# Performance work log

Measured on AMD Instinct MI355X. Metric: run time of the kernel, lower is better.

Reference implementation:

```python
import jax, jax.numpy as jnp
import numpy as np

N_NODES = 50000
N_EDGES = 400000
N_GRAPHS = 256
D = 200
N_STEPS = 6


def setup_inputs() -> dict:
    key = jax.random.key(0)
    ks = jax.random.split(key, 10)
    s = 1.0 / np.sqrt(D)
    x = jax.random.normal(ks[0], (N_NODES, D), dtype=jnp.float32)
    edge_index = jax.random.randint(ks[1], (2, N_EDGES), 0, N_NODES, dtype=jnp.int64)
    batch = jnp.sort(jax.random.randint(ks[2], (N_NODES,), 0, N_GRAPHS, dtype=jnp.int64))
    ggnn_weight = jax.random.uniform(ks[3], (N_STEPS, D, D), jnp.float32, -s, s)
    w_ih = jax.random.uniform(ks[4], (3 * D, D), jnp.float32, -s, s)
    w_hh = jax.random.uniform(ks[5], (3 * D, D), jnp.float32, -s, s)
    b_ih = jax.random.uniform(ks[6], (3 * D,), jnp.float32, -s, s)
    b_hh = jax.random.uniform(ks[7], (3 * D,), jnp.float32, -s, s)
    cls_w = jax.random.uniform(ks[8], (2, D), jnp.float32, -s, s)
    cls_b = jax.random.uniform(ks[9], (2,), jnp.float32, -s, s)
    return {"x": x, "edge_index": edge_index, "batch": batch,
            "ggnn_weight": ggnn_weight, "w_ih": w_ih, "w_hh": w_hh,
            "b_ih": b_ih, "b_hh": b_hh, "cls_w": cls_w, "cls_b": cls_b}


def _gru_cell(m, h, w_ih, w_hh, b_ih, b_hh):
    gi = m @ w_ih.T + b_ih            # [N, 3D]
    gh = h @ w_hh.T + b_hh            # [N, 3D]
    i_r, i_z, i_n = jnp.split(gi, 3, axis=-1)
    h_r, h_z, h_n = jnp.split(gh, 3, axis=-1)
    r = jax.nn.sigmoid(i_r + h_r)
    z = jax.nn.sigmoid(i_z + h_z)
    n = jnp.tanh(i_n + r * h_n)
    return (1.0 - z) * n + z * h


def reference(x, edge_index, batch, ggnn_weight, w_ih, w_hh, b_ih, b_hh, cls_w, cls_b):
    src, dst = edge_index[0], edge_index[1]

    def step(h, W):
        m = h @ W                                        # [N, D]
        agg = jax.ops.segment_sum(m[src], dst, num_segments=N_NODES)  # scatter-add
        return _gru_cell(agg, h, w_ih, w_hh, b_ih, b_hh), None

    h, _ = jax.lax.scan(step, x, ggnn_weight)
    h = jax.nn.relu(h)
    pooled = jax.ops.segment_max(h, batch, num_segments=N_GRAPHS)    # [G, D]
    logits = pooled @ cls_w.T + cls_b                                # [G, 2]
    return jax.nn.sigmoid(logits)
```

## Files before the change

### kernel.cpp

```cpp
#include <hip/hip_runtime.h>
#include <cstdint>
#include <cstddef>

#define NN 50000
#define NE 400000
#define NG 256
#define DIM 200
#define NSTEPS 6

typedef unsigned int uint;
typedef unsigned short ushort;
typedef __attribute__((ext_vector_type(8))) short short8;
typedef __attribute__((ext_vector_type(4))) float f32x4;

#define GLL16(gsrc, ldst)                                                        \
  __builtin_amdgcn_global_load_lds(                                              \
      (const __attribute__((address_space(1))) void*)(gsrc),                     \
      (__attribute__((address_space(3))) void*)(ldst), 16, 0, 0)

__device__ __forceinline__ float bfu(ushort u) { return __uint_as_float((uint)u << 16); }
__device__ __forceinline__ uint packf(float v) {
  uint u = __float_as_uint(v);
  uint t = u + 0x7fffu + ((u >> 16) & 1u);
  uint hb = t & 0xffff0000u;
  float lo = v - __uint_as_float(hb);
  uint ul = __float_as_uint(lo);
  uint t2 = ul + 0x7fffu + ((ul >> 16) & 1u);
  return hb | (t2 >> 16);
}
__device__ __forceinline__ uint packf_tr(float v) {
  uint u = __float_as_uint(v);
  uint t = u + 0x7fffu + ((u >> 16) & 1u);
  uint hb = t & 0xffff0000u;
  float lo = v - __uint_as_float(hb);
  return hb | (__float_as_uint(lo) >> 16);
}
__device__ __forceinline__ ushort bf16rn(float v) {
  uint u = __float_as_uint(v);
  return (ushort)((u + 0x7fffu + ((u >> 16) & 1u)) >> 16);
}
__device__ __forceinline__ float fsig(float x) {
  return __builtin_amdgcn_rcpf(1.f + __expf(-x));
}
__device__ __forceinline__ float ftanh(float x) {
  return 1.f - 2.f * __builtin_amdgcn_rcpf(__expf(2.f * x) + 1.f);
}

__global__ void k_zero_i32(int* __restrict__ p, int n) {
  for (int i = blockIdx.x * blockDim.x + threadIdx.x; i < n; i += gridDim.x * blockDim.x)
    p[i] = 0;
}
__global__ void k_zero_f32(float* __restrict__ p, int n) {
  for (int i = blockIdx.x * blockDim.x + threadIdx.x; i < n; i += gridDim.x * blockDim.x)
    p[i] = 0.f;
}
__global__ void k_hist(const int* __restrict__ dst, int* __restrict__ cnt, int nE) {
  int e = blockIdx.x * blockDim.x + threadIdx.x;
  if (e < nE) atomicAdd(&cnt[dst[e]], 1);
}

__global__ __launch_bounds__(256) void k_scan_blk(const int* __restrict__ cnt,
                                                  int* __restrict__ incl,
                                                  int* __restrict__ bsum, int n) {
  __shared__ int buf[256];
  int i = blockIdx.x * 256 + threadIdx.x;
  int v = (i < n) ? cnt[i] : 0;
  buf[threadIdx.x] = v;
  __syncthreads();
#pragma unroll
  for (int d = 1; d < 256; d <<= 1) {
    int t = (threadIdx.x >= d) ? buf[threadIdx.x - d] : 0;
    __syncthreads();
    buf[threadIdx.x] += t;
    __syncthreads();
  }
  if (i < n) incl[i] = buf[threadIdx.x];
  if (threadIdx.x == 255) bsum[blockIdx.x] = buf[255];
}
__global__ __launch_bounds__(256) void k_scan_top(int* __restrict__ bsum, int nb) {
  __shared__ int buf[256];
  int v = (threadIdx.x < nb) ? bsum[threadIdx.x] : 0;
  buf[threadIdx.x] = v;
  __syncthreads();
#pragma unroll
  for (int d = 1; d < 256; d <<= 1) {
    int t = (threadIdx.x >= d) ? buf[threadIdx.x - d] : 0;
    __syncthreads();
    buf[threadIdx.x] += t;
    __syncthreads();
  }
  if (threadIdx.x < nb) bsum[threadIdx.x] = buf[threadIdx.x] - v;
}
__global__ __launch_bounds__(256) void k_scan_fin(const int* __restrict__ cnt,
                                                  const int* __restrict__ incl,
                                                  const int* __restrict__ bsum,
                                                  int* __restrict__ off,
                                                  int* __restrict__ cursor, int n) {
  int i = blockIdx.x * 256 + threadIdx.x;
  if (i < n) {
    int o = incl[i] + bsum[blockIdx.x];
    off[i + 1] = o;
    cursor[i] = o - cnt[i];
  }
  if (i == 0) off[0] = 0;
}

__global__ void k_scatter(const int* __restrict__ dst, const int* __restrict__ src,
                          int* __restrict__ cursor, int* __restrict__ slist, int nE) {
  int e = blockIdx.x * blockDim.x + threadIdx.x;
  if (e < nE) {
    int d = dst[e];
    int pos = atomicAdd(&cursor[d], 1);
    slist[pos] = src[e];
  }
}

__global__ void k_pack_split(const float* __restrict__ x, ushort* __restrict__ hHi,
                             ushort* __restrict__ hLo, int n8) {
  for (int i = blockIdx.x * blockDim.x + threadIdx.x; i < n8;
       i += gridDim.x * blockDim.x) {
    const float* s = x + (size_t)i * 8;
    uint hi[4], lo[4];
#pragma unroll
    for (int j = 0; j < 4; ++j) {
      uint w0 = packf(s[j * 2]), w1 = packf(s[j * 2 + 1]);
      hi[j] = (w0 >> 16) | (w1 & 0xffff0000u);
      lo[j] = (w0 & 0xffffu) | (w1 << 16);
    }
    *reinterpret_cast<uint4*>(hHi + (size_t)i * 8) = make_uint4(hi[0], hi[1], hi[2], hi[3]);
    *reinterpret_cast<uint4*>(hLo + (size_t)i * 8) = make_uint4(lo[0], lo[1], lo[2], lo[3]);
  }
}

__global__ void k_pack_bf(const float* __restrict__ in, ushort* __restrict__ out, int n) {
  for (int i = blockIdx.x * blockDim.x + threadIdx.x; i < n; i += gridDim.x * blockDim.x)
    out[i] = bf16rn(in[i]);
}

#define GBM 64
#define GBN 64
#define GBK 8
__global__ __launch_bounds__(256) void k_gemm_wc(const float* __restrict__ gg,
                                                 const float* __restrict__ w_ih,
                                                 ushort* __restrict__ wcB) {
  __shared__ __align__(16) float As[GBK][GBM];
  __shared__ __align__(16) float Bs[GBK][GBN];
  int s = blockIdx.z;
  const float* A = gg + (size_t)s * DIM * DIM;
  ushort* out = wcB + (size_t)s * 3 * DIM * DIM;
  int tid = threadIdx.x;
  int row0 = blockIdx.y * GBM;
  int col0 = blockIdx.x * GBN;
  int ty = tid >> 4, tx = tid & 15;
  float acc[4][4] = {};
  for (int k0 = 0; k0 < DIM; k0 += GBK) {
    {
      int r = tid >> 2;
      int kk = (tid & 3) * 2;
      int gr = row0 + r;
      float2 v = make_float2(0.f, 0.f);
      if (gr < DIM) v = *reinterpret_cast<const float2*>(&A[(size_t)gr * DIM + k0 + kk]);
      As[kk][r] = v.x; As[kk + 1][r] = v.y;
    }
    {
      int n = tid >> 2;
      int kk = (tid & 3) * 2;
      int gn = col0 + n;
      float2 v = *reinterpret_cast<const float2*>(&w_ih[(size_t)gn * DIM + k0 + kk]);
      Bs[kk][n] = v.x; Bs[kk + 1][n] = v.y;
    }
    __syncthreads();
#pragma unroll
    for (int k = 0; k < GBK; ++k) {
      float4 av = *reinterpret_cast<const float4*>(&As[k][ty * 4]);
      float4 bv = *reinterpret_cast<const float4*>(&Bs[k][tx * 4]);
      float a[4] = {av.x, av.y, av.z, av.w};
      float b[4] = {bv.x, bv.y, bv.z, bv.w};
#pragma unroll
      for (int i = 0; i < 4; ++i)
#pragma unroll
        for (int j = 0; j < 4; ++j) acc[i][j] += a[i] * b[j];
    }
    __syncthreads();
  }
#pragma unroll
  for (int i = 0; i < 4; ++i) {
    int r = row0 + ty * 4 + i;
    if (r >= DIM) continue;
#pragma unroll
    for (int j = 0; j < 4; ++j) {
      int c = col0 + tx * 4 + j;
      out[(size_t)c * DIM + r] = bf16rn(acc[i][j]);
    }
  }
}

__global__ __launch_bounds__(256) void k_aggregate_hi(const ushort* __restrict__ hHi,
                                                      const int* __restrict__ off,
                                                      const int* __restrict__ slist,
                                                      ushort* __restrict__ aggHi) {
  int wid = blockIdx.x * 4 + (threadIdx.x >> 6);
  int half = (threadIdx.x >> 5) & 1;
  int node = wid * 2 + half;
  int lane32 = threadIdx.x & 31;
  bool nok = node < NN;
  bool act = (lane32 < 25) && nok;
  const uint4* hb = reinterpret_cast<const uint4*>(hHi);
  float a[8] = {};
  int beg = 0, end = 0;
  if (nok) { beg = off[node]; end = off[node + 1]; }
  int p = beg;
#define ACC8(q)                                                   \
  {                                                               \
    a[0] += __uint_as_float((q).x << 16);                         \
    a[1] += __uint_as_float((q).x & 0xffff0000u);                 \
    a[2] += __uint_as_float((q).y << 16);                         \
    a[3] += __uint_as_float((q).y & 0xffff0000u);                 \
    a[4] += __uint_as_float((q).z << 16);                         \
    a[5] += __uint_as_float((q).z & 0xffff0000u);                 \
    a[6] += __uint_as_float((q).w << 16);                         \
    a[7] += __uint_as_float((q).w & 0xffff0000u);                 \
  }
  for (; p + 7 < end; p += 8) {
    uint4 q[8];
    if (act) {
#pragma unroll
      for (int e = 0; e < 8; ++e) q[e] = hb[(size_t)slist[p + e] * 25 + lane32];
#pragma unroll
      for (int e = 0; e < 8; ++e) ACC8(q[e])
    }
  }
  for (; p + 3 < end; p += 4) {
    uint4 q[4];
    if (act) {
#pragma unroll
      for (int e = 0; e < 4; ++e) q[e] = hb[(size_t)slist[p + e] * 25 + lane32];
#pragma unroll
      for (int e = 0; e < 4; ++e) ACC8(q[e])
    }
  }
  for (; p < end; ++p) {
    int s = slist[p];
    if (act) {
      uint4 q = hb[(size_t)s * 25 + lane32];
      ACC8(q)
    }
  }
#undef ACC8
  if (act) {
    uint w[4];
#pragma unroll
    for (int j = 0; j < 4; ++j)
      w[j] = (uint)bf16rn(a[j * 2]) | ((uint)bf16rn(a[j * 2 + 1]) << 16);
    reinterpret_cast<uint4*>(aggHi)[(size_t)node * 25 + lane32] =
        make_uint4(w[0], w[1], w[2], w[3]);
  }
}

#define NPAN 391
#define PPC 3
#define NCHK 131
#define NCOLB 7
#define GRIDF 917

#define MFMA16(a, b, c) __builtin_amdgcn_mfma_f32_16x16x32_bf16(a, b, c, 0, 0, 0)

__global__ __launch_bounds__(256, 2) void k_fused_mfma(
    const ushort* __restrict__ aggHi, const ushort* __restrict__ hHi,
    const ushort* __restrict__ hLo,
    const ushort* __restrict__ wcB, const ushort* __restrict__ whB,
    const float* __restrict__ b_ih, const float* __restrict__ b_hh,
    ushort* __restrict__ hnHi, ushort* __restrict__ hnLo) {
  __shared__ uint4 Bb[6][25][32];

  int tid = threadIdx.x;
  int lane = tid & 63;
  int wv = tid >> 6;
  int lr = lane & 15;
  int kc = lane >> 4;

  int x = blockIdx.x & 7, ii = blockIdx.x >> 3;
  int work = (x < 5 ? x * 115 : 575 + (x - 5) * 114) + ii;
  int chunk = work / NCOLB;
  int col = work - chunk * NCOLB;
  int cc0 = col * 32;

  int c0 = cc0 + lr;
  int c1 = c0 + 16;
  bool c0ok = c0 < DIM, c1ok = c1 < DIM;
  int c0c = c0ok ? c0 : DIM - 1;
  int c1c = c1ok ? c1 : DIM - 1;

  float bias[2][6];
#pragma unroll
  for (int ct = 0; ct < 2; ++ct) {
    int c = ct ? c1c : c0c;
    bias[ct][0] = b_ih[c];           bias[ct][1] = b_ih[DIM + c];
    bias[ct][2] = b_ih[2 * DIM + c]; bias[ct][3] = b_hh[c];
    bias[ct][4] = b_hh[DIM + c];     bias[ct][5] = b_hh[2 * DIM + c];
  }

  {
    uint4* BbF = &Bb[0][0][0];
    for (int i2 = 0; i2 < 19; ++i2) {
      int u = tid + i2 * 256;
      if (u < 4800) {
        int mat = u / 800;
        int rem = u - mat * 800;
        int ch = rem >> 5;
        int c = rem & 31;
        int gc = cc0 + c; if (gc > 199) gc = 199;
        const ushort* wsrc = (mat & 1) ? whB : wcB;
        GLL16(wsrc + (size_t)((mat >> 1) * DIM + gc) * DIM + ch * 8, BbF + u);
      }
    }
  }
  __syncthreads();

  for (int j = 0; j < PPC; ++j) {
    int p = chunk * PPC + j;
    if (p >= NPAN) break;
    int prow0 = p * 128;
    int r0 = prow0 + wv * 32 + lr;
    int r1 = r0 + 16;
    int rc0 = r0 < NN ? r0 : NN - 1;
    int rc1 = r1 < NN ? r1 : NN - 1;
    const ushort* a0 = aggHi + (size_t)rc0 * DIM;
    const ushort* a1 = aggHi + (size_t)rc1 * DIM;
    const ushort* h0 = hHi + (size_t)rc0 * DIM;
    const ushort* h1 = hHi + (size_t)rc1 * DIM;

    uint rbase[2][4];
    bool rok[2][4];
#pragma unroll
    for (int rf = 0; rf < 2; ++rf)
#pragma unroll
      for (int qq = 0; qq < 4; ++qq) {
        int r_ = prow0 + wv * 32 + rf * 16 + kc * 4 + qq;
        rok[rf][qq] = r_ < NN;
        rbase[rf][qq] = (uint)(r_ < NN ? r_ : NN - 1) * DIM;
      }

    f32x4 acc[3][2][2][2] = {};
    short8 aq[4][2][2];
    ushort hvh[2][2][4], hvl[2][2][4];

#define LDA(d, t)                                                              \
  {                                                                            \
    const bool v_ = ((t) < 6) || (kc == 0);                                    \
    const int of_ = v_ ? ((t) * 32 + kc * 8) : 0;                              \
    const short8 z_ = {0, 0, 0, 0, 0, 0, 0, 0};                                \
    aq[d][0][0] = v_ ? *reinterpret_cast<const short8*>(a0 + of_) : z_;        \
    aq[d][0][1] = v_ ? *reinterpret_cast<const short8*>(a1 + of_) : z_;        \
    aq[d][1][0] = v_ ? *reinterpret_cast<const short8*>(h0 + of_) : z_;        \
    aq[d][1][1] = v_ ? *reinterpret_cast<const short8*>(h1 + of_) : z_;        \
  }

    LDA(0, 0)
    LDA(1, 1)
    LDA(2, 2)
#pragma unroll
    for (int t = 0; t < 7; ++t) {
      const int cur = t & 3;
      if (t < 4) LDA((t + 3) & 3, t + 3)
      if (t == 5) {
#pragma unroll
        for (int ct = 0; ct < 2; ++ct) {
          int cc = ct ? c1c : c0c;
#pragma unroll
          for (int rf = 0; rf < 2; ++rf)
#pragma unroll
            for (int qq = 0; qq < 4; ++qq) {
              uint base = rbase[rf][qq] + cc;
              hvh[ct][rf][qq] = hHi[base];
              hvl[ct][rf][qq] = hLo[base];
            }
        }
      }
      int bch = t * 4 + kc; if (bch > 24) bch = 24;
      __builtin_amdgcn_s_setprio(1);
#pragma unroll
      for (int g = 0; g < 3; ++g) {
#pragma unroll
        for (int ct = 0; ct < 2; ++ct) {
          short8 b1 = *reinterpret_cast<const short8*>(&Bb[g * 2 + 0][bch][ct * 16 + lr]);
          short8 b2 = *reinterpret_cast<const short8*>(&Bb[g * 2 + 1][bch][ct * 16 + lr]);
#pragma unroll
          for (int rf = 0; rf < 2; ++rf) {
            acc[g][0][rf][ct] = MFMA16(aq[cur][0][rf], b1, acc[g][0][rf][ct]);
            acc[g][1][rf][ct] = MFMA16(aq[cur][1][rf], b2, acc[g][1][rf][ct]);
          }
        }
      }
      __builtin_amdgcn_s_setprio(0);
    }
#undef LDA

#pragma unroll
    for (int ct = 0; ct < 2; ++ct) {
      if (!(ct ? c1ok : c0ok)) continue;
      int cc = ct ? c1 : c0;
#pragma unroll
      for (int rf = 0; rf < 2; ++rf) {
#pragma unroll
        for (int qq = 0; qq < 4; ++qq) {
          if (!rok[rf][qq]) continue;
          uint base = rbase[rf][qq] + cc;
          float gir = acc[0][0][rf][ct][qq] + bias[ct][0];
          float giz = acc[1][0][rf][ct][qq] + bias[ct][1];
          float gin = acc[2][0][rf][ct][qq] + bias[ct][2];
          float ghr = acc[0][1][rf][ct][qq] + bias[ct][3];
          float ghz = acc[1][1][rf][ct][qq] + bias[ct][4];
          float ghn = acc[2][1][rf][ct][qq] + bias[ct][5];
          float rr = fsig(gir + ghr);
          float zz = fsig(giz + ghz);
          float nn = ftanh(gin + rr * ghn);
          float hv = bfu(hvh[ct][rf][qq]) + bfu(hvl[ct][rf][qq]);
          uint w = packf_tr(fmaf(zz, hv - nn, nn));
          hnHi[base] = (ushort)(w >> 16);
          hnLo[base] = (ushort)(w & 0xffffu);
        }
      }
    }
  }
}

__global__ __launch_bounds__(256) void k_pool(const ushort* __restrict__ hHi,
                                              const ushort* __restrict__ hLo,
                                              const int* __restrict__ batch,
                                              float* __restrict__ pooled) {
  int i = blockIdx.x;
  int j = threadIdx.x;
  if (j < DIM) {
    int g = batch[i];
    size_t base = (size_t)i * DIM + j;
    float v = bfu(hHi[base]) + bfu(hLo[base]);
    v = v > 0.f ? v : 0.f;
    atomicMax((int*)&pooled[(size_t)g * DIM + j], __float_as_int(v));
  }
}

__global__ __launch_bounds__(256) void k_classify(const float* __restrict__ pooled,
                                                  const float* __restrict__ w,
                                                  const float* __restrict__ b,
                                                  float* __restrict__ out) {
  __shared__ float r0[256], r1[256];
  int g = blockIdx.x;
  int j = threadIdx.x;
  float p = (j < DIM) ? pooled[(size_t)g * DIM + j] : 0.f;
  r0[j] = (j < DIM) ? p * w[j] : 0.f;
  r1[j] = (j < DIM) ? p * w[DIM + j] : 0.f;
  __syncthreads();
  for (int d = 128; d > 0; d >>= 1) {
    if (j < d) { r0[j] += r0[j + d]; r1[j] += r1[j + d]; }
    __syncthreads();
  }
  if (j == 0) {
    out[g * 2 + 0] = 1.f / (1.f + expf(-(r0[0] + b[0])));
    out[g * 2 + 1] = 1.f / (1.f + expf(-(r1[0] + b[1])));
  }
}

extern "C" void kernel_launch(void* const* d_in, const int* in_sizes, int n_in,
                              void* d_out, int out_size, void* d_ws, size_t ws_size,
                              hipStream_t stream) {
  const float* x = (const float*)d_in[0];
  const int* edge_index = (const int*)d_in[1];
  const int* batch = (const int*)d_in[2];
  const float* ggnn_w = (const float*)d_in[3];
  const float* w_ih = (const float*)d_in[4];
  const float* w_hh = (const float*)d_in[5];
  const float* b_ih = (const float*)d_in[6];
  const float* b_hh = (const float*)d_in[7];
  const float* cls_w = (const float*)d_in[8];
  const float* cls_b = (const float*)d_in[9];
  float* out = (float*)d_out;

  const int* src = edge_index;
  const int* dst = edge_index + NE;

  char* wsb = (char*)d_ws;
  size_t off = 0;
  auto alloc = [&](size_t bytes) -> void* {
    void* p = wsb + off;
    off += (bytes + 255) & ~(size_t)255;
    return p;
  };
  ushort* hHiA = (ushort*)alloc((size_t)NN * DIM * 2);
  ushort* hLoA = (ushort*)alloc((size_t)NN * DIM * 2);
  ushort* hHiB = (ushort*)alloc((size_t)NN * DIM * 2);
  ushort* hLoB = (ushort*)alloc((size_t)NN * DIM * 2);
  ushort* aggHi = (ushort*)alloc((size_t)NN * DIM * 2);
  ushort* wcB = (ushort*)alloc((size_t)NSTEPS * 3 * DIM * DIM * 2);
  ushort* whB = (ushort*)alloc((size_t)3 * DIM * DIM * 2);
  float* pooled = (float*)alloc((size_t)NG * DIM * 4);
  int* indeg = (int*)alloc((size_t)NN * 4);
  int* offs = (int*)alloc((size_t)(NN + 1) * 4);
  int* incl = (int*)alloc((size_t)NN * 4);
  int* bsum = (int*)alloc((size_t)256 * 4);
  int* cursor = (int*)alloc((size_t)NN * 4);
  int* slist = (int*)alloc((size_t)NE * 4);
  if (off > ws_size) return;

  const int NB = (NN + 255) / 256;

  k_pack_split<<<2048, 256, 0, stream>>>(x, hHiA, hLoA, NN * DIM / 8);

  k_zero_i32<<<196, 256, 0, stream>>>(indeg, NN);
  k_hist<<<(NE + 255) / 256, 256, 0, stream>>>(dst, indeg, NE);
  k_scan_blk<<<NB, 256, 0, stream>>>(indeg, incl, bsum, NN);
  k_scan_top<<<1, 256, 0, stream>>>(bsum, NB);
  k_scan_fin<<<NB, 256, 0, stream>>>(indeg, incl, bsum, offs, cursor, NN);
  k_scatter<<<(NE + 255) / 256, 256, 0, stream>>>(dst, src, cursor, slist, NE);

  {
    dim3 g((3 * DIM + GBN - 1) / GBN, (DIM + GBM - 1) / GBM, NSTEPS);
    k_gemm_wc<<<g, 256, 0, stream>>>(ggnn_w, w_ih, wcB);
    k_pack_bf<<<512, 256, 0, stream>>>(w_hh, whB, 3 * DIM * DIM);
  }

  ushort* hHic = hHiA;
  ushort* hLoc = hLoA;
  ushort* hHin = hHiB;
  ushort* hLon = hLoB;
  for (int s = 0; s < NSTEPS; ++s) {
    k_aggregate_hi<<<(NN / 2 + 3) / 4, 256, 0, stream>>>(hHic, offs, slist, aggHi);
    k_fused_mfma<<<GRIDF, 256, 0, stream>>>(aggHi, hHic, hLoc,
                                            wcB + (size_t)s * 3 * DIM * DIM,
                                            whB, b_ih, b_hh, hHin, hLon);
    ushort* t;
    t = hHic; hHic = hHin; hHin = t;
    t = hLoc; hLoc = hLon; hLon = t;
  }

  k_zero_f32<<<200, 256, 0, stream>>>(pooled, NG * DIM);
  k_pool<<<NN, 256, 0, stream>>>(hHic, hLoc, batch, pooled);
  k_classify<<<NG, 256, 0, stream>>>(pooled, cls_w, cls_b, out);
}
```

Measured before the change: 640.4 us.

## Fuse pooling into last GRU step, fold bias into MFMA, store fp32 hidden state

Makes the last fused GRU step apply ReLU and atomicMax directly into pooled, which removes the separate pool kernel and its read of the final hidden state. Folds the biases into the MFMA by adding an extra K chunk: a ones column in A and bf16 bias rows in the LDS B tile. Replaces the hi/lo bf16 split of the hidden state with an fp32 copy plus a bf16 copy, and reads x directly as the first step's fp32 state. The biases are now rounded to bf16, so accuracy drops slightly, and per-element atomics in the last step may contend.

```diff
diff --git a/kernel.cpp b/kernel.cpp
--- a/kernel.cpp
+++ b/kernel.cpp
@@ -19,22 +19,6 @@
       (__attribute__((address_space(3))) void*)(ldst), 16, 0, 0)
 
 __device__ __forceinline__ float bfu(ushort u) { return __uint_as_float((uint)u << 16); }
-__device__ __forceinline__ uint packf(float v) {
-  uint u = __float_as_uint(v);
-  uint t = u + 0x7fffu + ((u >> 16) & 1u);
-  uint hb = t & 0xffff0000u;
-  float lo = v - __uint_as_float(hb);
-  uint ul = __float_as_uint(lo);
-  uint t2 = ul + 0x7fffu + ((ul >> 16) & 1u);
-  return hb | (t2 >> 16);
-}
-__device__ __forceinline__ uint packf_tr(float v) {
-  uint u = __float_as_uint(v);
-  uint t = u + 0x7fffu + ((u >> 16) & 1u);
-  uint hb = t & 0xffff0000u;
-  float lo = v - __uint_as_float(hb);
-  return hb | (__float_as_uint(lo) >> 16);
-}
 __device__ __forceinline__ ushort bf16rn(float v) {
   uint u = __float_as_uint(v);
   return (ushort)((u + 0x7fffu + ((u >> 16) & 1u)) >> 16);
@@ -115,26 +99,35 @@
   }
 }
 
-__global__ void k_pack_split(const float* __restrict__ x, ushort* __restrict__ hHi,
-                             ushort* __restrict__ hLo, int n8) {
+__global__ void k_pack_hi(const float* __restrict__ x, ushort* __restrict__ hHi, int n8) {
   for (int i = blockIdx.x * blockDim.x + threadIdx.x; i < n8;
        i += gridDim.x * blockDim.x) {
     const float* s = x + (size_t)i * 8;
-    uint hi[4], lo[4];
-#pragma unroll
-    for (int j = 0; j < 4; ++j) {
-      uint w0 = packf(s[j * 2]), w1 = packf(s[j * 2 + 1]);
-      hi[j] = (w0 >> 16) | (w1 & 0xffff0000u);
-      lo[j] = (w0 & 0xffffu) | (w1 << 16);
-    }
-    *reinterpret_cast<uint4*>(hHi + (size_t)i * 8) = make_uint4(hi[0], hi[1], hi[2], hi[3]);
-    *reinterpret_cast<uint4*>(hLo + (size_t)i * 8) = make_uint4(lo[0], lo[1], lo[2], lo[3]);
+    uint w[4];
+#pragma unroll
+    for (int j = 0; j < 4; ++j)
+      w[j] = (uint)bf16rn(s[j * 2]) | ((uint)bf16rn(s[j * 2 + 1]) << 16);
+    *reinterpret_cast<uint4*>(hHi + (size_t)i * 8) = make_uint4(w[0], w[1], w[2], w[3]);
   }
 }
 
 __global__ void k_pack_bf(const float* __restrict__ in, ushort* __restrict__ out, int n) {
   for (int i = blockIdx.x * blockDim.x + threadIdx.x; i < n; i += gridDim.x * blockDim.x)
     out[i] = bf16rn(in[i]);
+}
+
+__global__ void k_prep_bias(const float* __restrict__ b_ih, const float* __restrict__ b_hh,
+                            ushort* __restrict__ bstg) {
+  int idx = blockIdx.x * blockDim.x + threadIdx.x;
+  if (idx < 6 * DIM) {
+    int mat = idx / DIM, c = idx - mat * DIM;
+    int g = mat >> 1;
+    float v = (mat & 1) ? b_hh[g * DIM + c] : b_ih[g * DIM + c];
+    ushort* d = bstg + (size_t)idx * 8;
+    d[0] = bf16rn(v);
+#pragma unroll
+    for (int j = 1; j < 8; ++j) d[j] = 0;
+  }
 }
 
 #define GBM 64
@@ -265,13 +258,15 @@
 
 #define MFMA16(a, b, c) __builtin_amdgcn_mfma_f32_16x16x32_bf16(a, b, c, 0, 0, 0)
 
+template <bool LAST>
 __global__ __launch_bounds__(256, 2) void k_fused_mfma(
     const ushort* __restrict__ aggHi, const ushort* __restrict__ hHi,
-    const ushort* __restrict__ hLo,
+    const float* __restrict__ hS,
     const ushort* __restrict__ wcB, const ushort* __restrict__ whB,
-    const float* __restrict__ b_ih, const float* __restrict__ b_hh,
-    ushort* __restrict__ hnHi, ushort* __restrict__ hnLo) {
-  __shared__ uint4 Bb[6][25][32];
+    const ushort* __restrict__ bstg,
+    ushort* __restrict__ hnHi, float* __restrict__ hnS,
+    const int* __restrict__ batch, float* __restrict__ pooled) {
+  __shared__ uint4 Bb[6][26][32];
 
   int tid = threadIdx.x;
   int lane = tid & 63;
@@ -291,27 +286,22 @@
   int c0c = c0ok ? c0 : DIM - 1;
   int c1c = c1ok ? c1 : DIM - 1;
 
-  float bias[2][6];
-#pragma unroll
-  for (int ct = 0; ct < 2; ++ct) {
-    int c = ct ? c1c : c0c;
-    bias[ct][0] = b_ih[c];           bias[ct][1] = b_ih[DIM + c];
-    bias[ct][2] = b_ih[2 * DIM + c]; bias[ct][3] = b_hh[c];
-    bias[ct][4] = b_hh[DIM + c];     bias[ct][5] = b_hh[2 * DIM + c];
-  }
-
   {
     uint4* BbF = &Bb[0][0][0];
-    for (int i2 = 0; i2 < 19; ++i2) {
+    for (int i2 = 0; i2 < 20; ++i2) {
       int u = tid + i2 * 256;
-      if (u < 4800) {
-        int mat = u / 800;
-        int rem = u - mat * 800;
+      if (u < 4992) {
+        int mat = u / 832;
+        int rem = u - mat * 832;
         int ch = rem >> 5;
         int c = rem & 31;
         int gc = cc0 + c; if (gc > 199) gc = 199;
-        const ushort* wsrc = (mat & 1) ? whB : wcB;
-        GLL16(wsrc + (size_t)((mat >> 1) * DIM + gc) * DIM + ch * 8, BbF + u);
+        if (ch < 25) {
+          const ushort* wsrc = (mat & 1) ? whB : wcB;
+          GLL16(wsrc + (size_t)(((mat >> 1) * DIM) + gc) * DIM + ch * 8, BbF + u);
+        } else {
+          GLL16(bstg + (size_t)(mat * DIM + gc) * 8, BbF + u);
+        }
       }
     }
   }
@@ -331,6 +321,7 @@
     const ushort* h1 = hHi + (size_t)rc1 * DIM;
 
     uint rbase[2][4];
+    int rcl2[2][4];
     bool rok[2][4];
 #pragma unroll
     for (int rf = 0; rf < 2; ++rf)
@@ -338,22 +329,36 @@
       for (int qq = 0; qq < 4; ++qq) {
         int r_ = prow0 + wv * 32 + rf * 16 + kc * 4 + qq;
         rok[rf][qq] = r_ < NN;
-        rbase[rf][qq] = (uint)(r_ < NN ? r_ : NN - 1) * DIM;
+        int rc = r_ < NN ? r_ : NN - 1;
+        rcl2[rf][qq] = rc;
+        rbase[rf][qq] = (uint)rc * DIM;
       }
 
     f32x4 acc[3][2][2][2] = {};
     short8 aq[4][2][2];
-    ushort hvh[2][2][4], hvl[2][2][4];
+    float hvf[2][2][4];
+    int bidx[2][4];
 
 #define LDA(d, t)                                                              \
   {                                                                            \
-    const bool v_ = ((t) < 6) || (kc == 0);                                    \
-    const int of_ = v_ ? ((t) * 32 + kc * 8) : 0;                              \
-    const short8 z_ = {0, 0, 0, 0, 0, 0, 0, 0};                                \
-    aq[d][0][0] = v_ ? *reinterpret_cast<const short8*>(a0 + of_) : z_;        \
-    aq[d][0][1] = v_ ? *reinterpret_cast<const short8*>(a1 + of_) : z_;        \
-    aq[d][1][0] = v_ ? *reinterpret_cast<const short8*>(h0 + of_) : z_;        \
-    aq[d][1][1] = v_ ? *reinterpret_cast<const short8*>(h1 + of_) : z_;        \
+    if ((t) < 6) {                                                             \
+      const int of_ = (t) * 32 + kc * 8;                                       \
+      aq[d][0][0] = *reinterpret_cast<const short8*>(a0 + of_);                \
+      aq[d][0][1] = *reinterpret_cast<const short8*>(a1 + of_);                \
+      aq[d][1][0] = *reinterpret_cast<const short8*>(h0 + of_);                \
+      aq[d][1][1] = *reinterpret_cast<const short8*>(h1 + of_);                \
+    } else if (kc == 0) {                                                      \
+      aq[d][0][0] = *reinterpret_cast<const short8*>(a0 + 192);                \
+      aq[d][0][1] = *reinterpret_cast<const short8*>(a1 + 192);                \
+      aq[d][1][0] = *reinterpret_cast<const short8*>(h0 + 192);                \
+      aq[d][1][1] = *reinterpret_cast<const short8*>(h1 + 192);                \
+    } else {                                                                   \
+      const short8 z_ = {0, 0, 0, 0, 0, 0, 0, 0};                              \
+      const short8 o_ = {(short)0x3F80, 0, 0, 0, 0, 0, 0, 0};                  \
+      short8 v_ = (kc == 1) ? o_ : z_;                                         \
+      aq[d][0][0] = v_; aq[d][0][1] = v_;                                      \
+      aq[d][1][0] = v_; aq[d][1][1] = v_;                                      \
+    }                                                                          \
   }
 
     LDA(0, 0)
@@ -365,19 +370,15 @@
       if (t < 4) LDA((t + 3) & 3, t + 3)
       if (t == 5) {
 #pragma unroll
-        for (int ct = 0; ct < 2; ++ct) {
-          int cc = ct ? c1c : c0c;
-#pragma unroll
-          for (int rf = 0; rf < 2; ++rf)
-#pragma unroll
-            for (int qq = 0; qq < 4; ++qq) {
-              uint base = rbase[rf][qq] + cc;
-              hvh[ct][rf][qq] = hHi[base];
-              hvl[ct][rf][qq] = hLo[base];
-            }
-        }
+        for (int rf = 0; rf < 2; ++rf)
+#pragma unroll
+          for (int qq = 0; qq < 4; ++qq) {
+            hvf[0][rf][qq] = hS[rbase[rf][qq] + c0c];
+            hvf[1][rf][qq] = hS[rbase[rf][qq] + c1c];
+            if (LAST) bidx[rf][qq] = batch[rcl2[rf][qq]];
+          }
       }
-      int bch = t * 4 + kc; if (bch > 24) bch = 24;
+      int bch = t * 4 + kc; if (bch >= 26) bch = 24;
       __builtin_amdgcn_s_setprio(1);
 #pragma unroll
       for (int g = 0; g < 3; ++g) {
@@ -406,37 +407,27 @@
         for (int qq = 0; qq < 4; ++qq) {
           if (!rok[rf][qq]) continue;
           uint base = rbase[rf][qq] + cc;
-          float gir = acc[0][0][rf][ct][qq] + bias[ct][0];
-          float giz = acc[1][0][rf][ct][qq] + bias[ct][1];
-          float gin = acc[2][0][rf][ct][qq] + bias[ct][2];
-          float ghr = acc[0][1][rf][ct][qq] + bias[ct][3];
-          float ghz = acc[1][1][rf][ct][qq] + bias[ct][4];
-          float ghn = acc[2][1][rf][ct][qq] + bias[ct][5];
+          float gir = acc[0][0][rf][ct][qq];
+          float giz = acc[1][0][rf][ct][qq];
+          float gin = acc[2][0][rf][ct][qq];
+          float ghr = acc[0][1][rf][ct][qq];
+          float ghz = acc[1][1][rf][ct][qq];
+          float ghn = acc[2][1][rf][ct][qq];
           float rr = fsig(gir + ghr);
           float zz = fsig(giz + ghz);
           float nn = ftanh(gin + rr * ghn);
-          float hv = bfu(hvh[ct][rf][qq]) + bfu(hvl[ct][rf][qq]);
-          uint w = packf_tr(fmaf(zz, hv - nn, nn));
-          hnHi[base] = (ushort)(w >> 16);
-          hnLo[base] = (ushort)(w & 0xffffu);
+          float hv = hvf[ct][rf][qq];
+          float v = fmaf(zz, hv - nn, nn);
+          if (LAST) {
+            v = v > 0.f ? v : 0.f;
+            atomicMax((int*)&pooled[(size_t)bidx[rf][qq] * DIM + cc], __float_as_int(v));
+          } else {
+            hnS[base] = v;
+            hnHi[base] = bf16rn(v);
+          }
         }
       }
     }
-  }
-}
-
-__global__ __launch_bounds__(256) void k_pool(const ushort* __restrict__ hHi,
-                                              const ushort* __restrict__ hLo,
-                                              const int* __restrict__ batch,
-                                              float* __restrict__ pooled) {
-  int i = blockIdx.x;
-  int j = threadIdx.x;
-  if (j < DIM) {
-    int g = batch[i];
-    size_t base = (size_t)i * DIM + j;
-    float v = bfu(hHi[base]) + bfu(hLo[base]);
-    v = v > 0.f ? v : 0.f;
-    atomicMax((int*)&pooled[(size_t)g * DIM + j], __float_as_int(v));
   }
 }
 
@@ -487,12 +478,13 @@
     return p;
   };
   ushort* hHiA = (ushort*)alloc((size_t)NN * DIM * 2);
-  ushort* hLoA = (ushort*)alloc((size_t)NN * DIM * 2);
   ushort* hHiB = (ushort*)alloc((size_t)NN * DIM * 2);
-  ushort* hLoB = (ushort*)alloc((size_t)NN * DIM * 2);
+  float* hSA = (float*)alloc((size_t)NN * DIM * 4);
+  float* hSB = (float*)alloc((size_t)NN * DIM * 4);
   ushort* aggHi = (ushort*)alloc((size_t)NN * DIM * 2);
   ushort* wcB = (ushort*)alloc((size_t)NSTEPS * 3 * DIM * DIM * 2);
   ushort* whB = (ushort*)alloc((size_t)3 * DIM * DIM * 2);
+  ushort* bstg = (ushort*)alloc((size_t)6 * DIM * 8 * 2);
   float* pooled = (float*)alloc((size_t)NG * DIM * 4);
   int* indeg = (int*)alloc((size_t)NN * 4);
   int* offs = (int*)alloc((size_t)(NN + 1) * 4);
@@ -504,7 +496,7 @@
 
   const int NB = (NN + 255) / 256;
 
-  k_pack_split<<<2048, 256, 0, stream>>>(x, hHiA, hLoA, NN * DIM / 8);
+  k_pack_hi<<<2048, 256, 0, stream>>>(x, hHiA, NN * DIM / 8);
 
   k_zero_i32<<<196, 256, 0, stream>>>(indeg, NN);
   k_hist<<<(NE + 255) / 256, 256, 0, stream>>>(dst, indeg, NE);
@@ -517,23 +509,29 @@
     dim3 g((3 * DIM + GBN - 1) / GBN, (DIM + GBM - 1) / GBM, NSTEPS);
     k_gemm_wc<<<g, 256, 0, stream>>>(ggnn_w, w_ih, wcB);
     k_pack_bf<<<512, 256, 0, stream>>>(w_hh, whB, 3 * DIM * DIM);
-  }
-
-  ushort* hHic = hHiA;
-  ushort* hLoc = hLoA;
+    k_prep_bias<<<5, 256, 0, stream>>>(b_ih, b_hh, bstg);
+  }
+
+  k_zero_f32<<<200, 256, 0, stream>>>(pooled, NG * DIM);
+
+  const ushort* hHic = hHiA;
   ushort* hHin = hHiB;
-  ushort* hLon = hLoB;
+  const float* hSc = x;
+  float* hSn = hSA;
   for (int s = 0; s < NSTEPS; ++s) {
     k_aggregate_hi<<<(NN / 2 + 3) / 4, 256, 0, stream>>>(hHic, offs, slist, aggHi);
-    k_fused_mfma<<<GRIDF, 256, 0, stream>>>(aggHi, hHic, hLoc,
-                                            wcB + (size_t)s * 3 * DIM * DIM,
-                                            whB, b_ih, b_hh, hHin, hLon);
-    ushort* t;
-    t = hHic; hHic = hHin; hHin = t;
-    t = hLoc; hLoc = hLon; hLon = t;
-  }
-
-  k_zero_f32<<<200, 256, 0, stream>>>(pooled, NG * DIM);
-  k_pool<<<NN, 256, 0, stream>>>(hHic, hLoc, batch, pooled);
+    const ushort* wc = wcB + (size_t)s * 3 * DIM * DIM;
+    if (s == NSTEPS - 1) {
+      k_fused_mfma<true><<<GRIDF, 256, 0, stream>>>(aggHi, hHic, hSc, wc, whB, bstg,
+                                                    hHin, hSn, batch, pooled);
+    } else {
+      k_fused_mfma<false><<<GRIDF, 256, 0, stream>>>(aggHi, hHic, hSc, wc, whB, bstg,
+                                                     hHin, hSn, batch, pooled);
+      const ushort* th = hHic; hHic = hHin; hHin = (ushort*)th;
+      hSc = hSn;
+      hSn = (hSn == hSA) ? hSB : hSA;
+    }
+  }
+
   k_classify<<<NG, 256, 0, stream>>>(pooled, cls_w, cls_b, out);
 }
```

Measured after the change: 700.7 us. 1.09x slower.
